# Kernel optimization log

Measured on AMD Instinct MI355X. Metric: run time of the kernel, lower is better.

## Reference

```python
import jax, jax.numpy as jnp
import numpy as np

# Module constants (Calculator __init__ scalars)
IXY = 1.0      # self.ixy
HX = 10.0      # self.hx
ALPHA = 2.0    # self.alpha
C = 1.0        # self.c
DIM = 4096     # self.dim (== len(lambdas) == len(gammas))
B = 8192       # batch of betas


def setup_inputs() -> dict:
    key = jax.random.key(0)
    kb, kl, kg = jax.random.split(key, 3)
    # betas in [2.5, DIM-0.5] so k_beta = floor(beta-1) is in [1, DIM-1]
    betas = 2.5 + jax.random.uniform(kb, (B,), dtype=jnp.float32) * (DIM - 3.0)
    # lambdas in (0.05, 0.95): eigen-like values strictly inside (0,1)
    lambdas = 0.05 + 0.9 * jax.random.uniform(kl, (DIM,), dtype=jnp.float32)
    # gammas ~ U(0,1)/DIM: small positive weights (keeps exp(2*ixt/n_I) bounded)
    gammas = jax.random.uniform(kg, (DIM,), dtype=jnp.float32) / DIM
    return {"betas": betas, "lambdas": lambdas, "gammas": gammas}


def reference(betas, lambdas, gammas):
    dim = lambdas.shape[0]
    dt = betas.dtype

    # ---- beta_placer: k = floor((1 - lambda)^-1 - 1), lambda = 1 - beta^-1 ----
    lam = 1.0 - 1.0 / betas
    k_frac = 1.0 / (1.0 - lam) - 1.0
    k_beta = jnp.floor(k_frac).astype(jnp.int32)                 # [B]

    # ---- ixt ----
    kbf = k_beta.astype(dt)
    lambda_max = 1.0 - 1.0 / (kbf + 1.0)                         # [B]
    kk = jnp.arange(1, dim + 1, dtype=dt)                        # [dim] (k = 1..dim)
    lam_k = 1.0 - 1.0 / (kk + 1.0)                               # [dim]
    mask = jnp.arange(dim)[None, :] < k_beta[:, None]            # [B, dim] ragged mask
    # k_multiplier_ixt: log(lambda_max*(1-lambda_k)/(lambda_k*(1-lambda_max)))
    ratio = (lambda_max[:, None] * (1.0 - lam_k)[None, :]) / (
        lam_k[None, :] * (1.0 - lambda_max)[:, None])
    multipliers = jnp.where(mask, jnp.log(ratio), 0.0)           # [B, dim]
    ixt = jnp.sum(gammas[None, :] * multipliers)                 # scalar

    # ---- chechik_term ----
    maskf = mask.astype(dt)
    mg_un = gammas[None, :] * maskf                              # masked gammas (unnorm.)
    n_I = jnp.sum(mg_un)
    mg = mg_un / n_I                                             # normalized, sums to 1
    # prod(pow(masked_lambdas, mg)) with 0^0 = 1 on masked-out entries
    # == exp(sum_{mask} mg * log(lambdas))
    gm_term = jnp.exp(jnp.sum(jnp.where(mask, mg * jnp.log(lambdas)[None, :], 0.0)))
    gm_comp_term = jnp.exp(jnp.sum(jnp.where(mask, mg * jnp.log1p(-lambdas)[None, :], 0.0)))
    exp_term = jnp.exp(2.0 * ixt / n_I)
    log_term = -n_I / 2.0 * jnp.log(gm_comp_term + exp_term * gm_term)

    # ---- ity / iy / rhs ----
    ity = ixt + log_term
    rhs = 1.0 - ity / IXY

    # ---- lhs ----
    lhs_1 = 1.0 - ixt / HX
    lhs_1 = jnp.where(lhs_1 < 0, jnp.abs(lhs_1) * 20.0, lhs_1)
    lhs = C * jnp.power(lhs_1, ALPHA)

    return (rhs, lhs)
```

## Files before the change

### kernel.cpp

```cpp
#include <hip/hip_runtime.h>
#include <math.h>

#define DIM 4096
#define BATCH 8192
#define NT 1024
#define NWAVES (NT / 64)
#define RPT (BATCH / NT)

__global__ __launch_bounds__(NT)
void calc_kernel(const float* __restrict__ betas,
                 const float* __restrict__ lambdas,
                 const float* __restrict__ gammas,
                 float* __restrict__ out)
{
    __shared__ float4 s4[DIM];
    __shared__ float4 ovl4[NWAVES];
    __shared__ float4 red4[NWAVES];

    const int t = threadIdx.x;
    const int lane = t & 63;
    const int wave = t >> 6;
    const int j0 = t * 4;

    const float4 la4 = *reinterpret_cast<const float4*>(lambdas + j0);
    const float4 ga4 = *reinterpret_cast<const float4*>(gammas + j0);
    const float4* b4p = reinterpret_cast<const float4*>(betas);
    float4 bv[RPT / 4];
    #pragma unroll
    for (int r = 0; r < RPT / 4; ++r) bv[r] = b4p[r * NT + t];

    float bet[RPT] = { bv[0].x, bv[0].y, bv[0].z, bv[0].w,
                       bv[1].x, bv[1].y, bv[1].z, bv[1].w };
    int   K[RPT];
    float lk[RPT];
    #pragma unroll
    for (int r = 0; r < RPT; ++r) {
        float beta = bet[r];
        float lamb = 1.0f - 1.0f / beta;
        float kf   = 1.0f / (1.0f - lamb) - 1.0f;
        int k = (int)floorf(kf);
        k = min(max(k, 1), DIM - 1);
        K[r]  = k;
        lk[r] = __logf((float)k);
    }

    float las[4] = { la4.x, la4.y, la4.z, la4.w };
    float gas[4] = { ga4.x, ga4.y, ga4.z, ga4.w };
    float e[4][4];
    float tot0 = 0.f, tot1 = 0.f, tot2 = 0.f, tot3 = 0.f;
    #pragma unroll
    for (int i = 0; i < 4; ++i) {
        float g = gas[i];
        float l = las[i];
        float v0 = g;
        float v1 = g * __logf((float)(j0 + i + 1));
        float v2 = g * __logf(l);
        float v3 = g * __logf(1.0f - l);
        e[i][0] = v0; e[i][1] = v1; e[i][2] = v2; e[i][3] = v3;
        tot0 += v0; tot1 += v1; tot2 += v2; tot3 += v3;
    }

    float i0 = tot0, i1 = tot1, i2 = tot2, i3 = tot3;
    #pragma unroll
    for (int off = 1; off < 64; off <<= 1) {
        float y0 = __shfl_up(i0, off, 64);
        float y1 = __shfl_up(i1, off, 64);
        float y2 = __shfl_up(i2, off, 64);
        float y3 = __shfl_up(i3, off, 64);
        if (lane >= off) { i0 += y0; i1 += y1; i2 += y2; i3 += y3; }
    }
    if (lane == 63) ovl4[wave] = make_float4(i0, i1, i2, i3);
    __syncthreads();

    float b0 = i0 - tot0, b1 = i1 - tot1, b2 = i2 - tot2, b3 = i3 - tot3;
    for (int w = 0; w < wave; ++w) {
        float4 o = ovl4[w];
        b0 += o.x; b1 += o.y; b2 += o.z; b3 += o.w;
    }
    #pragma unroll
    for (int i = 0; i < 4; ++i) {
        b0 += e[i][0]; b1 += e[i][1]; b2 += e[i][2]; b3 += e[i][3];
        s4[j0 + i] = make_float4(b0, b1, b2, b3);
    }
    __syncthreads();

    float a0 = 0.f, a1 = 0.f, a2 = 0.f, a3 = 0.f;
    #pragma unroll
    for (int r = 0; r < RPT; ++r) {
        float4 p = s4[K[r] - 1];
        a0 += lk[r] * p.x - p.y;
        a1 += p.x;
        a2 += p.z;
        a3 += p.w;
    }

    #pragma unroll
    for (int off = 32; off > 0; off >>= 1) {
        a0 += __shfl_down(a0, off, 64);
        a1 += __shfl_down(a1, off, 64);
        a2 += __shfl_down(a2, off, 64);
        a3 += __shfl_down(a3, off, 64);
    }
    if (lane == 0) red4[wave] = make_float4(a0, a1, a2, a3);
    __syncthreads();
    if (t == 0) {
        float ixt = 0.f, nI = 0.f, Sl = 0.f, Sl1 = 0.f;
        #pragma unroll
        for (int w = 0; w < NWAVES; ++w) {
            float4 rv = red4[w];
            ixt += rv.x; nI += rv.y; Sl += rv.z; Sl1 += rv.w;
        }
        float inv_nI = 1.0f / nI;
        float gm_term  = __expf(Sl * inv_nI);
        float gm_comp  = __expf(Sl1 * inv_nI);
        float exp_term = __expf(2.0f * ixt * inv_nI);
        float log_term = -nI * 0.5f * __logf(gm_comp + exp_term * gm_term);
        float ity = ixt + log_term;
        float rhs = 1.0f - ity;
        float l1  = 1.0f - ixt * 0.1f;
        if (l1 < 0.0f) l1 = fabsf(l1) * 20.0f;
        out[0] = rhs;
        out[1] = l1 * l1;
    }
}

extern "C" void kernel_launch(void* const* d_in, const int* in_sizes, int n_in,
                              void* d_out, int out_size, void* d_ws, size_t ws_size,
                              hipStream_t stream) {
    const float* betas   = (const float*)d_in[0];
    const float* lambdas = (const float*)d_in[1];
    const float* gammas  = (const float*)d_in[2];
    calc_kernel<<<1, NT, 0, stream>>>(betas, lambdas, gammas, (float*)d_out);
}
```

Baseline: 12.70 us.

## Replace prefix-sum gather with histogram of k_beta and suffix-count scan

Instead of building a prefix sum over gammas and gathering it per beta, each thread atomically adds a packed (count, fixed-point log k) value into a shared histogram bin indexed by k_beta. A reversed scan over the bins then gives, for each dimension j, how many betas cover it, and each term is weighted by those counts. The float4 prefix array and its random gather go away, in exchange for 64-bit shared atomics, an extra barrier and a fixed-point approximation of log k at 1/16384 resolution. The fixed-point log sum has to fit in 32 bits.

```diff
diff --git a/kernel.cpp b/kernel.cpp
--- a/kernel.cpp
+++ b/kernel.cpp
@@ -13,26 +13,28 @@
                  const float* __restrict__ gammas,
                  float* __restrict__ out)
 {
-    __shared__ float4 s4[DIM];
-    __shared__ float4 ovl4[NWAVES];
-    __shared__ float4 red4[NWAVES];
+    __shared__ unsigned long long hbin[DIM];
+    __shared__ uint2 wtot[NWAVES];
+    __shared__ float red[5][NWAVES];
 
     const int t = threadIdx.x;
     const int lane = t & 63;
     const int wave = t >> 6;
-    const int j0 = t * 4;
+    const int jb = DIM - 4 - 4 * t;
 
-    const float4 la4 = *reinterpret_cast<const float4*>(lambdas + j0);
-    const float4 ga4 = *reinterpret_cast<const float4*>(gammas + j0);
+    const float4 la4 = *reinterpret_cast<const float4*>(lambdas + jb);
+    const float4 ga4 = *reinterpret_cast<const float4*>(gammas + jb);
     const float4* b4p = reinterpret_cast<const float4*>(betas);
-    float4 bv[RPT / 4];
-    #pragma unroll
-    for (int r = 0; r < RPT / 4; ++r) bv[r] = b4p[r * NT + t];
+    const float4 bv0 = b4p[t];
+    const float4 bv1 = b4p[NT + t];
 
-    float bet[RPT] = { bv[0].x, bv[0].y, bv[0].z, bv[0].w,
-                       bv[1].x, bv[1].y, bv[1].z, bv[1].w };
-    int   K[RPT];
-    float lk[RPT];
+    uint4* hz = reinterpret_cast<uint4*>(hbin);
+    hz[2 * t]     = make_uint4(0u, 0u, 0u, 0u);
+    hz[2 * t + 1] = make_uint4(0u, 0u, 0u, 0u);
+
+    float bet[RPT] = { bv0.x, bv0.y, bv0.z, bv0.w, bv1.x, bv1.y, bv1.z, bv1.w };
+    unsigned long long incv[RPT];
+    int K[RPT];
     #pragma unroll
     for (int r = 0; r < RPT; ++r) {
         float beta = bet[r];
@@ -40,58 +42,68 @@
         float kf   = 1.0f / (1.0f - lamb) - 1.0f;
         int k = (int)floorf(kf);
         k = min(max(k, 1), DIM - 1);
-        K[r]  = k;
-        lk[r] = __logf((float)k);
+        K[r] = k;
+        unsigned int lkfix = __float2uint_rn(__logf((float)k) * 16384.0f);
+        incv[r] = (1ull << 32) | (unsigned long long)lkfix;
     }
 
-    float las[4] = { la4.x, la4.y, la4.z, la4.w };
-    float gas[4] = { ga4.x, ga4.y, ga4.z, ga4.w };
-    float e[4][4];
-    float tot0 = 0.f, tot1 = 0.f, tot2 = 0.f, tot3 = 0.f;
+    float lam_s[4] = { la4.w, la4.z, la4.y, la4.x };
+    float gam_s[4] = { ga4.w, ga4.z, ga4.y, ga4.x };
+    float e_g[4], e_gl[4], e_gA[4], e_gB[4];
     #pragma unroll
     for (int i = 0; i < 4; ++i) {
-        float g = gas[i];
-        float l = las[i];
-        float v0 = g;
-        float v1 = g * __logf((float)(j0 + i + 1));
-        float v2 = g * __logf(l);
-        float v3 = g * __logf(1.0f - l);
-        e[i][0] = v0; e[i][1] = v1; e[i][2] = v2; e[i][3] = v3;
-        tot0 += v0; tot1 += v1; tot2 += v2; tot3 += v3;
+        int j = jb + 3 - i;
+        float g = gam_s[i];
+        e_g[i]  = g;
+        e_gl[i] = g * __logf((float)(j + 1));
+        e_gA[i] = g * __logf(lam_s[i]);
+        e_gB[i] = g * __logf(1.0f - lam_s[i]);
     }
 
-    float i0 = tot0, i1 = tot1, i2 = tot2, i3 = tot3;
+    __syncthreads();
+
+    #pragma unroll
+    for (int r = 0; r < RPT; ++r)
+        atomicAdd(&hbin[K[r]], incv[r]);
+
+    __syncthreads();
+
+    const uint4 q0 = *reinterpret_cast<const uint4*>(&hbin[jb]);
+    const uint4 q1 = *reinterpret_cast<const uint4*>(&hbin[jb + 2]);
+    unsigned int cnt_s[4] = { q1.w, q1.y, q0.w, q0.y };
+    unsigned int lk_s[4]  = { q1.z, q1.x, q0.z, q0.x };
+
+    unsigned int tc = cnt_s[0] + cnt_s[1] + cnt_s[2] + cnt_s[3];
+    unsigned int tl = lk_s[0] + lk_s[1] + lk_s[2] + lk_s[3];
+
+    unsigned int ic = tc, il = tl;
     #pragma unroll
     for (int off = 1; off < 64; off <<= 1) {
-        float y0 = __shfl_up(i0, off, 64);
-        float y1 = __shfl_up(i1, off, 64);
-        float y2 = __shfl_up(i2, off, 64);
-        float y3 = __shfl_up(i3, off, 64);
-        if (lane >= off) { i0 += y0; i1 += y1; i2 += y2; i3 += y3; }
+        unsigned int yc = __shfl_up(ic, off, 64);
+        unsigned int yl = __shfl_up(il, off, 64);
+        if (lane >= off) { ic += yc; il += yl; }
     }
-    if (lane == 63) ovl4[wave] = make_float4(i0, i1, i2, i3);
+    if (lane == 63) wtot[wave] = make_uint2(ic, il);
     __syncthreads();
 
-    float b0 = i0 - tot0, b1 = i1 - tot1, b2 = i2 - tot2, b3 = i3 - tot3;
+    unsigned int bc = ic - tc, bl = il - tl;
     for (int w = 0; w < wave; ++w) {
-        float4 o = ovl4[w];
-        b0 += o.x; b1 += o.y; b2 += o.z; b3 += o.w;
+        uint2 wt = wtot[w];
+        bc += wt.x; bl += wt.y;
     }
+
+    float a0 = 0.f, a1 = 0.f, a2 = 0.f, a3 = 0.f, a4 = 0.f;
+    unsigned int rc = bc, rl = bl;
     #pragma unroll
     for (int i = 0; i < 4; ++i) {
-        b0 += e[i][0]; b1 += e[i][1]; b2 += e[i][2]; b3 += e[i][3];
-        s4[j0 + i] = make_float4(b0, b1, b2, b3);
-    }
-    __syncthreads();
-
-    float a0 = 0.f, a1 = 0.f, a2 = 0.f, a3 = 0.f;
-    #pragma unroll
-    for (int r = 0; r < RPT; ++r) {
-        float4 p = s4[K[r] - 1];
-        a0 += lk[r] * p.x - p.y;
-        a1 += p.x;
-        a2 += p.z;
-        a3 += p.w;
+        float cntf = (float)rc;
+        float slkf = (float)rl * (1.0f / 16384.0f);
+        a0 += e_g[i]  * slkf;
+        a1 += e_gl[i] * cntf;
+        a2 += e_g[i]  * cntf;
+        a3 += e_gA[i] * cntf;
+        a4 += e_gB[i] * cntf;
+        rc += cnt_s[i]; rl += lk_s[i];
     }
 
     #pragma unroll
@@ -100,23 +112,28 @@
         a1 += __shfl_down(a1, off, 64);
         a2 += __shfl_down(a2, off, 64);
         a3 += __shfl_down(a3, off, 64);
+        a4 += __shfl_down(a4, off, 64);
     }
-    if (lane == 0) red4[wave] = make_float4(a0, a1, a2, a3);
+    if (lane == 0) {
+        red[0][wave] = a0; red[1][wave] = a1; red[2][wave] = a2;
+        red[3][wave] = a3; red[4][wave] = a4;
+    }
     __syncthreads();
     if (t == 0) {
-        float ixt = 0.f, nI = 0.f, Sl = 0.f, Sl1 = 0.f;
+        float s0 = 0.f, s1 = 0.f, s2 = 0.f, s3 = 0.f, s4 = 0.f;
         #pragma unroll
         for (int w = 0; w < NWAVES; ++w) {
-            float4 rv = red4[w];
-            ixt += rv.x; nI += rv.y; Sl += rv.z; Sl1 += rv.w;
+            s0 += red[0][w]; s1 += red[1][w]; s2 += red[2][w];
+            s3 += red[3][w]; s4 += red[4][w];
         }
+        float ixt = s0 - s1;
+        float nI  = s2;
         float inv_nI = 1.0f / nI;
-        float gm_term  = __expf(Sl * inv_nI);
-        float gm_comp  = __expf(Sl1 * inv_nI);
+        float gm_term  = __expf(s3 * inv_nI);
+        float gm_comp  = __expf(s4 * inv_nI);
         float exp_term = __expf(2.0f * ixt * inv_nI);
         float log_term = -nI * 0.5f * __logf(gm_comp + exp_term * gm_term);
-        float ity = ixt + log_term;
-        float rhs = 1.0f - ity;
+        float rhs = 1.0f - (ixt + log_term);
         float l1  = 1.0f - ixt * 0.1f;
         if (l1 < 0.0f) l1 = fabsf(l1) * 20.0f;
         out[0] = rhs;
```

Measured after the change: 12.76 us. About the same (+0.5%).

## Split single-block kernel into multi-block prefix table and parallel join kernels

Applied to the files above, without the earlier changes.

Replaces the single 1024-thread block with two launches. The first builds chunked prefix sums of the gamma-weighted logs across 16 blocks and writes them to workspace memory. The second gathers per-beta prefix values across 32 blocks, combines chunk offsets, and reduces with global atomics plus a last-block ticket to compute the outputs. The aim is to spread work over more compute units, at the cost of a second launch, global-memory round trips and atomics.

```diff
diff --git a/kernel.cpp b/kernel.cpp
--- a/kernel.cpp
+++ b/kernel.cpp
@@ -3,64 +3,39 @@
 
 #define DIM 4096
 #define BATCH 8192
-#define NT 1024
-#define NWAVES (NT / 64)
-#define RPT (BATCH / NT)
+#define NCHUNK 16
+#define CHUNK 256
+#define K2_BLOCKS 32
+#define K2_NT 256
 
-__global__ __launch_bounds__(NT)
-void calc_kernel(const float* __restrict__ betas,
-                 const float* __restrict__ lambdas,
-                 const float* __restrict__ gammas,
-                 float* __restrict__ out)
+#define TABLE_OFF  0
+#define CHUNK_OFF  (DIM * 16)
+#define ACC_OFF    (CHUNK_OFF + 256)
+#define TICKET_OFF (ACC_OFF + 16)
+
+__global__ __launch_bounds__(CHUNK)
+void k1_table(const float* __restrict__ lambdas,
+              const float* __restrict__ gammas,
+              float4* __restrict__ table,
+              float4* __restrict__ chunktot,
+              float* __restrict__ accs,
+              unsigned int* __restrict__ ticket)
 {
-    __shared__ float4 s4[DIM];
-    __shared__ float4 ovl4[NWAVES];
-    __shared__ float4 red4[NWAVES];
-
+    __shared__ float4 wv[CHUNK / 64];
     const int t = threadIdx.x;
+    const int b = blockIdx.x;
+    const int j = b * CHUNK + t;
     const int lane = t & 63;
     const int wave = t >> 6;
-    const int j0 = t * 4;
 
-    const float4 la4 = *reinterpret_cast<const float4*>(lambdas + j0);
-    const float4 ga4 = *reinterpret_cast<const float4*>(gammas + j0);
-    const float4* b4p = reinterpret_cast<const float4*>(betas);
-    float4 bv[RPT / 4];
-    #pragma unroll
-    for (int r = 0; r < RPT / 4; ++r) bv[r] = b4p[r * NT + t];
+    float g = gammas[j];
+    float l = lambdas[j];
+    float v0 = g;
+    float v1 = g * __logf((float)(j + 1));
+    float v2 = g * __logf(l);
+    float v3 = g * __logf(1.0f - l);
 
-    float bet[RPT] = { bv[0].x, bv[0].y, bv[0].z, bv[0].w,
-                       bv[1].x, bv[1].y, bv[1].z, bv[1].w };
-    int   K[RPT];
-    float lk[RPT];
-    #pragma unroll
-    for (int r = 0; r < RPT; ++r) {
-        float beta = bet[r];
-        float lamb = 1.0f - 1.0f / beta;
-        float kf   = 1.0f / (1.0f - lamb) - 1.0f;
-        int k = (int)floorf(kf);
-        k = min(max(k, 1), DIM - 1);
-        K[r]  = k;
-        lk[r] = __logf((float)k);
-    }
-
-    float las[4] = { la4.x, la4.y, la4.z, la4.w };
-    float gas[4] = { ga4.x, ga4.y, ga4.z, ga4.w };
-    float e[4][4];
-    float tot0 = 0.f, tot1 = 0.f, tot2 = 0.f, tot3 = 0.f;
-    #pragma unroll
-    for (int i = 0; i < 4; ++i) {
-        float g = gas[i];
-        float l = las[i];
-        float v0 = g;
-        float v1 = g * __logf((float)(j0 + i + 1));
-        float v2 = g * __logf(l);
-        float v3 = g * __logf(1.0f - l);
-        e[i][0] = v0; e[i][1] = v1; e[i][2] = v2; e[i][3] = v3;
-        tot0 += v0; tot1 += v1; tot2 += v2; tot3 += v3;
-    }
-
-    float i0 = tot0, i1 = tot1, i2 = tot2, i3 = tot3;
+    float i0 = v0, i1 = v1, i2 = v2, i3 = v3;
     #pragma unroll
     for (int off = 1; off < 64; off <<= 1) {
         float y0 = __shfl_up(i0, off, 64);
@@ -69,30 +44,62 @@
         float y3 = __shfl_up(i3, off, 64);
         if (lane >= off) { i0 += y0; i1 += y1; i2 += y2; i3 += y3; }
     }
-    if (lane == 63) ovl4[wave] = make_float4(i0, i1, i2, i3);
-    __syncthreads();
+    if (lane == 63) wv[wave] = make_float4(i0, i1, i2, i3);
 
-    float b0 = i0 - tot0, b1 = i1 - tot1, b2 = i2 - tot2, b3 = i3 - tot3;
-    for (int w = 0; w < wave; ++w) {
-        float4 o = ovl4[w];
-        b0 += o.x; b1 += o.y; b2 += o.z; b3 += o.w;
-    }
-    #pragma unroll
-    for (int i = 0; i < 4; ++i) {
-        b0 += e[i][0]; b1 += e[i][1]; b2 += e[i][2]; b3 += e[i][3];
-        s4[j0 + i] = make_float4(b0, b1, b2, b3);
+    if (b == 0) {
+        if (t < 4) accs[t] = 0.0f;
+        if (t == 4) *ticket = 0u;
     }
     __syncthreads();
 
-    float a0 = 0.f, a1 = 0.f, a2 = 0.f, a3 = 0.f;
     #pragma unroll
-    for (int r = 0; r < RPT; ++r) {
-        float4 p = s4[K[r] - 1];
-        a0 += lk[r] * p.x - p.y;
-        a1 += p.x;
-        a2 += p.z;
-        a3 += p.w;
+    for (int w = 0; w < CHUNK / 64; ++w) {
+        if (w < wave) {
+            float4 o = wv[w];
+            i0 += o.x; i1 += o.y; i2 += o.z; i3 += o.w;
+        }
     }
+    table[j] = make_float4(i0, i1, i2, i3);
+    if (t == CHUNK - 1) chunktot[b] = make_float4(i0, i1, i2, i3);
+}
+
+__global__ __launch_bounds__(K2_NT)
+void k2_join(const float* __restrict__ betas,
+             const float4* __restrict__ table,
+             const float4* __restrict__ chunktot,
+             float* __restrict__ accs,
+             unsigned int* __restrict__ ticket,
+             float* __restrict__ out)
+{
+    __shared__ float4 raw[NCHUNK];
+    __shared__ float4 red[K2_NT / 64];
+    const int t = threadIdx.x;
+    const int lane = t & 63;
+    const int wave = t >> 6;
+    const int tid = blockIdx.x * K2_NT + t;
+
+    if (t < NCHUNK) raw[t] = chunktot[t];
+
+    float beta = betas[tid];
+    float lamb = 1.0f - 1.0f / beta;
+    float kf   = 1.0f / (1.0f - lamb) - 1.0f;
+    int K = (int)floorf(kf);
+    K = min(max(K, 1), DIM - 1);
+    float lk = __logf((float)K);
+    __syncthreads();
+
+    const int c = (K - 1) >> 8;
+    float b0 = 0.f, b1 = 0.f, b2 = 0.f, b3 = 0.f;
+    for (int w = 0; w < c; ++w) {
+        float4 o = raw[w];
+        b0 += o.x; b1 += o.y; b2 += o.z; b3 += o.w;
+    }
+    float4 p = table[K - 1];
+    float G  = b0 + p.x;
+    float a0 = lk * G - (b1 + p.y);
+    float a1 = G;
+    float a2 = b2 + p.z;
+    float a3 = b3 + p.w;
 
     #pragma unroll
     for (int off = 32; off > 0; off >>= 1) {
@@ -101,26 +108,38 @@
         a2 += __shfl_down(a2, off, 64);
         a3 += __shfl_down(a3, off, 64);
     }
-    if (lane == 0) red4[wave] = make_float4(a0, a1, a2, a3);
+    if (lane == 0) red[wave] = make_float4(a0, a1, a2, a3);
     __syncthreads();
+
     if (t == 0) {
-        float ixt = 0.f, nI = 0.f, Sl = 0.f, Sl1 = 0.f;
+        float s0 = 0.f, s1 = 0.f, s2 = 0.f, s3 = 0.f;
         #pragma unroll
-        for (int w = 0; w < NWAVES; ++w) {
-            float4 rv = red4[w];
-            ixt += rv.x; nI += rv.y; Sl += rv.z; Sl1 += rv.w;
+        for (int w = 0; w < K2_NT / 64; ++w) {
+            float4 rv = red[w];
+            s0 += rv.x; s1 += rv.y; s2 += rv.z; s3 += rv.w;
         }
-        float inv_nI = 1.0f / nI;
-        float gm_term  = __expf(Sl * inv_nI);
-        float gm_comp  = __expf(Sl1 * inv_nI);
-        float exp_term = __expf(2.0f * ixt * inv_nI);
-        float log_term = -nI * 0.5f * __logf(gm_comp + exp_term * gm_term);
-        float ity = ixt + log_term;
-        float rhs = 1.0f - ity;
-        float l1  = 1.0f - ixt * 0.1f;
-        if (l1 < 0.0f) l1 = fabsf(l1) * 20.0f;
-        out[0] = rhs;
-        out[1] = l1 * l1;
+        atomicAdd(&accs[0], s0);
+        atomicAdd(&accs[1], s1);
+        atomicAdd(&accs[2], s2);
+        atomicAdd(&accs[3], s3);
+        __threadfence();
+        unsigned int old = atomicAdd(ticket, 1u);
+        if (old == K2_BLOCKS - 1) {
+            float ixt = atomicAdd(&accs[0], 0.0f);
+            float nI  = atomicAdd(&accs[1], 0.0f);
+            float Sl  = atomicAdd(&accs[2], 0.0f);
+            float Sl1 = atomicAdd(&accs[3], 0.0f);
+            float inv_nI = 1.0f / nI;
+            float gm_term  = __expf(Sl  * inv_nI);
+            float gm_comp  = __expf(Sl1 * inv_nI);
+            float exp_term = __expf(2.0f * ixt * inv_nI);
+            float log_term = -nI * 0.5f * __logf(gm_comp + exp_term * gm_term);
+            float rhs = 1.0f - (ixt + log_term);
+            float l1  = 1.0f - ixt * 0.1f;
+            if (l1 < 0.0f) l1 = fabsf(l1) * 20.0f;
+            out[0] = rhs;
+            out[1] = l1 * l1;
+        }
     }
 }
 
@@ -130,5 +149,13 @@
     const float* betas   = (const float*)d_in[0];
     const float* lambdas = (const float*)d_in[1];
     const float* gammas  = (const float*)d_in[2];
-    calc_kernel<<<1, NT, 0, stream>>>(betas, lambdas, gammas, (float*)d_out);
+    char* ws = (char*)d_ws;
+    float4* table          = (float4*)(ws + TABLE_OFF);
+    float4* chunktot       = (float4*)(ws + CHUNK_OFF);
+    float* accs            = (float*)(ws + ACC_OFF);
+    unsigned int* ticket   = (unsigned int*)(ws + TICKET_OFF);
+
+    k1_table<<<NCHUNK, CHUNK, 0, stream>>>(lambdas, gammas, table, chunktot, accs, ticket);
+    k2_join<<<K2_BLOCKS, K2_NT, 0, stream>>>(betas, table, chunktot, accs, ticket,
+                                             (float*)d_out);
 }
```

Measured after the change: 16.02 us. 26.1% more time.

## Split beta batch across eight cooperative blocks with grid sync reduction

Applied to the files above, without the earlier changes.

Moves from a single 1024-thread block to eight cooperative blocks, each handling one slice of the betas. Every block redundantly rebuilds the full prefix-sum table in shared memory. Partial sums go to workspace slots, and after a grid-wide sync block 0 does the final reduction and scalar math. This spreads the per-beta gather work across more CUs, but pays for cooperative launch overhead, a grid barrier, and the prefix scan being recomputed in every block.

```diff
diff --git a/kernel.cpp b/kernel.cpp
--- a/kernel.cpp
+++ b/kernel.cpp
@@ -1,16 +1,20 @@
 #include <hip/hip_runtime.h>
+#include <hip/hip_cooperative_groups.h>
 #include <math.h>
+
+namespace cg = cooperative_groups;
 
 #define DIM 4096
 #define BATCH 8192
+#define NB 8
 #define NT 1024
 #define NWAVES (NT / 64)
-#define RPT (BATCH / NT)
 
 __global__ __launch_bounds__(NT)
 void calc_kernel(const float* __restrict__ betas,
                  const float* __restrict__ lambdas,
                  const float* __restrict__ gammas,
+                 float4* __restrict__ slots,
                  float* __restrict__ out)
 {
     __shared__ float4 s4[DIM];
@@ -21,28 +25,17 @@
     const int lane = t & 63;
     const int wave = t >> 6;
     const int j0 = t * 4;
+    const int blk = blockIdx.x;
 
     const float4 la4 = *reinterpret_cast<const float4*>(lambdas + j0);
     const float4 ga4 = *reinterpret_cast<const float4*>(gammas + j0);
-    const float4* b4p = reinterpret_cast<const float4*>(betas);
-    float4 bv[RPT / 4];
-    #pragma unroll
-    for (int r = 0; r < RPT / 4; ++r) bv[r] = b4p[r * NT + t];
+    const float beta = betas[blk * NT + t];
 
-    float bet[RPT] = { bv[0].x, bv[0].y, bv[0].z, bv[0].w,
-                       bv[1].x, bv[1].y, bv[1].z, bv[1].w };
-    int   K[RPT];
-    float lk[RPT];
-    #pragma unroll
-    for (int r = 0; r < RPT; ++r) {
-        float beta = bet[r];
-        float lamb = 1.0f - 1.0f / beta;
-        float kf   = 1.0f / (1.0f - lamb) - 1.0f;
-        int k = (int)floorf(kf);
-        k = min(max(k, 1), DIM - 1);
-        K[r]  = k;
-        lk[r] = __logf((float)k);
-    }
+    float lamb = 1.0f - 1.0f / beta;
+    float kf   = 1.0f / (1.0f - lamb) - 1.0f;
+    int K = (int)floorf(kf);
+    K = min(max(K, 1), DIM - 1);
+    float lk = __logf((float)K);
 
     float las[4] = { la4.x, la4.y, la4.z, la4.w };
     float gas[4] = { ga4.x, ga4.y, ga4.z, ga4.w };
@@ -84,15 +77,11 @@
     }
     __syncthreads();
 
-    float a0 = 0.f, a1 = 0.f, a2 = 0.f, a3 = 0.f;
-    #pragma unroll
-    for (int r = 0; r < RPT; ++r) {
-        float4 p = s4[K[r] - 1];
-        a0 += lk[r] * p.x - p.y;
-        a1 += p.x;
-        a2 += p.z;
-        a3 += p.w;
-    }
+    float4 p = s4[K - 1];
+    float a0 = lk * p.x - p.y;
+    float a1 = p.x;
+    float a2 = p.z;
+    float a3 = p.w;
 
     #pragma unroll
     for (int off = 32; off > 0; off >>= 1) {
@@ -104,19 +93,31 @@
     if (lane == 0) red4[wave] = make_float4(a0, a1, a2, a3);
     __syncthreads();
     if (t == 0) {
-        float ixt = 0.f, nI = 0.f, Sl = 0.f, Sl1 = 0.f;
+        float s0 = 0.f, s1 = 0.f, s2 = 0.f, s3 = 0.f;
         #pragma unroll
         for (int w = 0; w < NWAVES; ++w) {
             float4 rv = red4[w];
-            ixt += rv.x; nI += rv.y; Sl += rv.z; Sl1 += rv.w;
+            s0 += rv.x; s1 += rv.y; s2 += rv.z; s3 += rv.w;
+        }
+        slots[blk] = make_float4(s0, s1, s2, s3);
+    }
+
+    cg::this_grid().sync();
+
+    if (blk == 0 && t == 0) {
+        __threadfence();
+        float ixt = 0.f, nI = 0.f, Sl = 0.f, Sl1 = 0.f;
+        #pragma unroll
+        for (int i = 0; i < NB; ++i) {
+            float4 v = slots[i];
+            ixt += v.x; nI += v.y; Sl += v.z; Sl1 += v.w;
         }
         float inv_nI = 1.0f / nI;
-        float gm_term  = __expf(Sl * inv_nI);
+        float gm_term  = __expf(Sl  * inv_nI);
         float gm_comp  = __expf(Sl1 * inv_nI);
         float exp_term = __expf(2.0f * ixt * inv_nI);
         float log_term = -nI * 0.5f * __logf(gm_comp + exp_term * gm_term);
-        float ity = ixt + log_term;
-        float rhs = 1.0f - ity;
+        float rhs = 1.0f - (ixt + log_term);
         float l1  = 1.0f - ixt * 0.1f;
         if (l1 < 0.0f) l1 = fabsf(l1) * 20.0f;
         out[0] = rhs;
@@ -130,5 +131,10 @@
     const float* betas   = (const float*)d_in[0];
     const float* lambdas = (const float*)d_in[1];
     const float* gammas  = (const float*)d_in[2];
-    calc_kernel<<<1, NT, 0, stream>>>(betas, lambdas, gammas, (float*)d_out);
+    float4* slots = (float4*)d_ws;
+    float*  out   = (float*)d_out;
+    void* args[] = { (void*)&betas, (void*)&lambdas, (void*)&gammas,
+                     (void*)&slots, (void*)&out };
+    hipLaunchCooperativeKernel((const void*)calc_kernel, dim3(NB), dim3(NT),
+                               args, 0, stream);
 }
```

New measurement: 32.89 us. +158.9%, slower.
